# Kernel tuning notes

Measured on AMD Instinct MI355X. Metric: run time of the kernel, lower is better.

Reference implementation:

```python
import jax, jax.numpy as jnp
import numpy as np
from jax import lax

BIG = 1.0e6  # sentinel distance when a row contains no foreground pixel


def _dist1d(fg):
    """Exact 1D distance (in pixels) to nearest True along the last axis.

    fg: bool [..., W]. Returns float32 [..., W]; BIG where no True in the row.
    """
    W = fg.shape[-1]
    idx = jnp.arange(W, dtype=jnp.int32)
    # nearest foreground index to the left (inclusive)
    last = lax.cummax(jnp.where(fg, idx, -1), axis=fg.ndim - 1)
    d_left = jnp.where(last >= 0, (idx - last).astype(jnp.float32), BIG)
    # nearest foreground to the right: same scan on the reversed row
    fr = fg[..., ::-1]
    lastr = lax.cummax(jnp.where(fr, idx, -1), axis=fg.ndim - 1)
    d_right = jnp.where(lastr >= 0, (idx - lastr).astype(jnp.float32), BIG)[..., ::-1]
    return jnp.minimum(d_left, d_right)


def _edt2d(gt):
    """Exact Euclidean distance transform: distance from each pixel to the
    nearest gt==1 pixel (== scipy.distance_transform_edt(1-gt)).

    gt: [B, H, W] int. Returns float32 [B, H, W].
    Separable decomposition: D2(i,w) = min_j (d_row(j,w)^2 + (i-j)^2).
    """
    H = gt.shape[1]
    d_row = _dist1d(gt > 0)            # [B, H, W] 1D distances along rows
    dr2 = d_row * d_row                # squared row distances
    i = jnp.arange(H, dtype=jnp.float32)
    offs = (i[:, None] - i[None, :]) ** 2            # [Hi, Hj]
    # [B, Hi, Hj, W] = dr2 broadcast over i  +  (i-j)^2 broadcast over b, w
    d2 = jnp.min(dr2[:, None, :, :] + offs[None, :, :, None], axis=2)
    return jnp.sqrt(d2)


def setup_inputs() -> dict:
    key = jax.random.key(0)
    k1, k2 = jax.random.split(key)
    B, C, H, W = 8, 1, 256, 256
    logits = jax.random.normal(k1, (B, C, H, W), dtype=jnp.float32)
    target = jax.random.randint(k2, (B, C, H, W), 0, 2, dtype=jnp.int32)
    return {"logits": logits, "target": target}


def reference(logits, target):
    prob = jax.nn.sigmoid(logits)                      # [B, 1, H, W]
    D_gt = _edt2d(target[:, 0, :, :])[:, None, :, :]   # [B, 1, H, W]
    return jnp.mean(prob * D_gt)
```

## Files before the change

### kernel.cpp

```cpp
#include <hip/hip_runtime.h>


#define BIGF 1000000.0f
#define BIG2 (BIGF * BIGF)

constexpr int B = 8;
constexpr int H = 256;
constexpr int W = 256;
constexpr int NPIX = B * H * W;

__device__ __forceinline__ float block_reduce_sum_256(float v) {
    #pragma unroll
    for (int off = 32; off > 0; off >>= 1)
        v += __shfl_down(v, off, 64);
    __shared__ float s[4];
    const int lane = threadIdx.x & 63;
    const int wid  = threadIdx.x >> 6;
    if (lane == 0) s[wid] = v;
    __syncthreads();
    if (wid == 0) {
        v = (lane < 4) ? s[lane] : 0.0f;
        v += __shfl_down(v, 2, 64);
        v += __shfl_down(v, 1, 64);
    }
    return v;
}

__device__ __forceinline__ void upd16(const float4 m, float j0,
                                      float n0, float n1, float n2, float n3,
                                      float& b0, float& b1, float& b2, float& b3) {
    const float j1 = j0 + 1.0f, j2 = j0 + 2.0f, j3 = j0 + 3.0f;
    {
        const float c0 = fmaf(n0, j0, m.x), c1 = fmaf(n0, j1, m.y);
        const float c2 = fmaf(n0, j2, m.z), c3 = fmaf(n0, j3, m.w);
        b0 = fminf(b0, fminf(fminf(c0, c1), fminf(c2, c3)));
    }
    {
        const float c0 = fmaf(n1, j0, m.x), c1 = fmaf(n1, j1, m.y);
        const float c2 = fmaf(n1, j2, m.z), c3 = fmaf(n1, j3, m.w);
        b1 = fminf(b1, fminf(fminf(c0, c1), fminf(c2, c3)));
    }
    {
        const float c0 = fmaf(n2, j0, m.x), c1 = fmaf(n2, j1, m.y);
        const float c2 = fmaf(n2, j2, m.z), c3 = fmaf(n2, j3, m.w);
        b2 = fminf(b2, fminf(fminf(c0, c1), fminf(c2, c3)));
    }
    {
        const float c0 = fmaf(n3, j0, m.x), c1 = fmaf(n3, j1, m.y);
        const float c2 = fmaf(n3, j2, m.z), c3 = fmaf(n3, j3, m.w);
        b3 = fminf(b3, fminf(fminf(c0, c1), fminf(c2, c3)));
    }
}

__global__ __launch_bounds__(256) void row_dist_kernel(
        const int* __restrict__ target, float* __restrict__ dr2) {
    __shared__ float s_q[4][256];
    const int lane = threadIdx.x & 63;
    const int wv   = threadIdx.x >> 6;
    const int row  = (blockIdx.x << 2) + wv;

    const int4 tv = *(const int4*)(target + row * W + (lane << 2));
    const float fj0 = (float)(lane << 2);
    const float fj1 = fj0 + 1.0f, fj2 = fj0 + 2.0f, fj3 = fj0 + 3.0f;
    float4 q;
    q.x = fmaf(fj0, fj0, tv.x > 0 ? 0.0f : BIG2);
    q.y = fmaf(fj1, fj1, tv.y > 0 ? 0.0f : BIG2);
    q.z = fmaf(fj2, fj2, tv.z > 0 ? 0.0f : BIG2);
    q.w = fmaf(fj3, fj3, tv.w > 0 ? 0.0f : BIG2);
    *(float4*)&s_q[wv][lane << 2] = q;
    __syncthreads();

    const float w0f = (float)lane,         w1f = (float)(lane + 64);
    const float w2f = (float)(lane + 128), w3f = (float)(lane + 192);
    const float n0 = -2.0f * w0f, n1 = -2.0f * w1f;
    const float n2 = -2.0f * w2f, n3 = -2.0f * w3f;
    float b0 = 4e12f, b1 = 4e12f, b2 = 4e12f, b3 = 4e12f;

    float fj = 0.0f;
    #pragma unroll 4
    for (int jv = 0; jv < 64; ++jv, fj += 4.0f) {
        const float4 m = *(const float4*)&s_q[wv][jv << 2];
        upd16(m, fj, n0, n1, n2, n3, b0, b1, b2, b3);
    }

    const int base = row * W + lane;
    dr2[base]       = fmaf(w0f, w0f, b0);
    dr2[base + 64]  = fmaf(w1f, w1f, b1);
    dr2[base + 128] = fmaf(w2f, w2f, b2);
    dr2[base + 192] = fmaf(w3f, w3f, b3);
}

__global__ __launch_bounds__(256) void col_pass_kernel(
        const float* __restrict__ logits, const float* __restrict__ dr2,
        float* __restrict__ partials) {
    __shared__ float s_q[4][256];
    const int t  = threadIdx.x;
    const int b  = blockIdx.x >> 6;
    const int w0 = (blockIdx.x & 63) << 2;

    const float4 v  = *(const float4*)(dr2 + (b * H + t) * W + w0);
    const float fj  = (float)t;
    const float fj2 = fj * fj;
    s_q[0][t] = fj2 + v.x;
    s_q[1][t] = fj2 + v.y;
    s_q[2][t] = fj2 + v.z;
    s_q[3][t] = fj2 + v.w;
    __syncthreads();

    const int lane = t & 63;
    const int wv   = t >> 6;
    const float i0f = (float)lane,         i1f = (float)(lane + 64);
    const float i2f = (float)(lane + 128), i3f = (float)(lane + 192);
    const float n0 = -2.0f * i0f, n1 = -2.0f * i1f;
    const float n2 = -2.0f * i2f, n3 = -2.0f * i3f;
    float b0 = 4e12f, b1 = 4e12f, b2 = 4e12f, b3 = 4e12f;

    float fjv = 0.0f;
    #pragma unroll 4
    for (int jv = 0; jv < 64; ++jv, fjv += 4.0f) {
        const float4 m = *(const float4*)&s_q[wv][jv << 2];
        upd16(m, fjv, n0, n1, n2, n3, b0, b1, b2, b3);
    }

    const int wcol = w0 + wv;
    const int base = (b * H + lane) * W + wcol;
    float acc;
    {
        const float dist = sqrtf(fmaf(i0f, i0f, b0));
        const float x = logits[base];
        acc = dist / (1.0f + expf(-x));
    }
    {
        const float dist = sqrtf(fmaf(i1f, i1f, b1));
        const float x = logits[base + 64 * W];
        acc += dist / (1.0f + expf(-x));
    }
    {
        const float dist = sqrtf(fmaf(i2f, i2f, b2));
        const float x = logits[base + 128 * W];
        acc += dist / (1.0f + expf(-x));
    }
    {
        const float dist = sqrtf(fmaf(i3f, i3f, b3));
        const float x = logits[base + 192 * W];
        acc += dist / (1.0f + expf(-x));
    }

    const float s = block_reduce_sum_256(acc);
    if (t == 0) partials[blockIdx.x] = s;
}

__global__ __launch_bounds__(256) void final_reduce_kernel(
        const float* __restrict__ partials, float* __restrict__ out,
        int n, float scale) {
    float v = 0.0f;
    for (int idx = threadIdx.x; idx < n; idx += 256)
        v += partials[idx];
    v = block_reduce_sum_256(v);
    if (threadIdx.x == 0) out[0] = v * scale;
}

extern "C" void kernel_launch(void* const* d_in, const int* in_sizes, int n_in,
                              void* d_out, int out_size, void* d_ws, size_t ws_size,
                              hipStream_t stream) {
    const float* logits = (const float*)d_in[0];
    const int*   target = (const int*)d_in[1];

    float* dr2      = (float*)d_ws;
    float* partials = dr2 + NPIX;

    row_dist_kernel<<<B * H / 4, 256, 0, stream>>>(target, dr2);
    col_pass_kernel<<<B * W / 4, 256, 0, stream>>>(logits, dr2, partials);
    final_reduce_kernel<<<1, 256, 0, stream>>>(partials, (float*)d_out,
                                               B * W / 4, 1.0f / (float)NPIX);
}
```

Measured before the change: 74.56 us.

## Replace brute-force row pass with wave scans; split column min and fuse reduction

The row pass no longer does an O(W^2) min-plus search. It computes exact 1D nearest-foreground distances with wavefront prefix max/min scans (shfl_up/shfl_down), then writes the squared distances. The column pass now handles two columns per block and splits the j range across wave pairs, combining partial minima through shared memory. This doubles the block count and coalesces the logits loads as float2. The final reduce kernel is removed: each block atomically adds its scaled sum into the output, which the row kernel zeroes first. That relies on kernel ordering, and float atomics make the result order-nondeterministic.

```diff
diff --git a/kernel.cpp b/kernel.cpp
--- a/kernel.cpp
+++ b/kernel.cpp
@@ -3,6 +3,7 @@
 
 #define BIGF 1000000.0f
 #define BIG2 (BIGF * BIGF)
+#define BIGI (1 << 20)
 
 constexpr int B = 8;
 constexpr int H = 256;
@@ -24,6 +25,65 @@
         v += __shfl_down(v, 1, 64);
     }
     return v;
+}
+
+__global__ __launch_bounds__(256) void row_dist_kernel(
+        const int* __restrict__ target, float* __restrict__ dr2,
+        float* __restrict__ out) {
+    if (blockIdx.x == 0 && threadIdx.x == 0) out[0] = 0.0f;
+
+    const int lane = threadIdx.x & 63;
+    const int wv   = threadIdx.x >> 6;
+    const int row  = (blockIdx.x << 2) + wv;
+    const int p0   = lane << 2;
+
+    const int4 tv = *(const int4*)(target + row * W + p0);
+
+    const int l0 = (tv.x > 0) ? p0     : -1;
+    const int l1 = (tv.y > 0) ? p0 + 1 : l0;
+    const int l2 = (tv.z > 0) ? p0 + 2 : l1;
+    const int l3 = (tv.w > 0) ? p0 + 3 : l2;
+    int v = l3;
+    #pragma unroll
+    for (int off = 1; off < 64; off <<= 1) {
+        const int u = __shfl_up(v, off, 64);
+        if (lane >= off) v = max(v, u);
+    }
+    int exv = __shfl_up(v, 1, 64);
+    if (lane == 0) exv = -1;
+    const int last0 = max(exv, l0), last1 = max(exv, l1);
+    const int last2 = max(exv, l2), last3 = max(exv, l3);
+
+    const int r3 = (tv.w > 0) ? p0 + 3 : BIGI;
+    const int r2 = (tv.z > 0) ? p0 + 2 : r3;
+    const int r1 = (tv.y > 0) ? p0 + 1 : r2;
+    const int r0 = (tv.x > 0) ? p0     : r1;
+    int s = r0;
+    #pragma unroll
+    for (int off = 1; off < 64; off <<= 1) {
+        const int u = __shfl_down(s, off, 64);
+        if (lane < 64 - off) s = min(s, u);
+    }
+    int exs = __shfl_down(s, 1, 64);
+    if (lane == 63) exs = BIGI;
+    const int nxt0 = min(exs, r0), nxt1 = min(exs, r1);
+    const int nxt2 = min(exs, r2), nxt3 = min(exs, r3);
+
+    const int dl0 = (last0 >= 0) ? p0     - last0 : BIGI;
+    const int dl1 = (last1 >= 0) ? p0 + 1 - last1 : BIGI;
+    const int dl2 = (last2 >= 0) ? p0 + 2 - last2 : BIGI;
+    const int dl3 = (last3 >= 0) ? p0 + 3 - last3 : BIGI;
+    const int d0 = min(dl0, nxt0 - p0);
+    const int d1 = min(dl1, nxt1 - (p0 + 1));
+    const int d2 = min(dl2, nxt2 - (p0 + 2));
+    const int d3 = min(dl3, nxt3 - (p0 + 3));
+
+    float4 o;
+    o.x = (d0 < W) ? (float)(d0 * d0) : BIG2;
+    o.y = (d1 < W) ? (float)(d1 * d1) : BIG2;
+    o.z = (d2 < W) ? (float)(d2 * d2) : BIG2;
+    o.w = (d3 < W) ? (float)(d3 * d3) : BIG2;
+    *(float4*)(dr2 + row * W + p0) = o;
 }
 
 __device__ __forceinline__ void upd16(const float4 m, float j0,
@@ -52,112 +112,62 @@
     }
 }
 
-__global__ __launch_bounds__(256) void row_dist_kernel(
-        const int* __restrict__ target, float* __restrict__ dr2) {
-    __shared__ float s_q[4][256];
-    const int lane = threadIdx.x & 63;
-    const int wv   = threadIdx.x >> 6;
-    const int row  = (blockIdx.x << 2) + wv;
+__global__ __launch_bounds__(256) void col_pass_kernel(
+        const float* __restrict__ logits, const float* __restrict__ dr2,
+        float* __restrict__ out) {
+    __shared__ float s_q[2][256];
+    __shared__ float s_part[4][256];
 
-    const int4 tv = *(const int4*)(target + row * W + (lane << 2));
-    const float fj0 = (float)(lane << 2);
-    const float fj1 = fj0 + 1.0f, fj2 = fj0 + 2.0f, fj3 = fj0 + 3.0f;
-    float4 q;
-    q.x = fmaf(fj0, fj0, tv.x > 0 ? 0.0f : BIG2);
-    q.y = fmaf(fj1, fj1, tv.y > 0 ? 0.0f : BIG2);
-    q.z = fmaf(fj2, fj2, tv.z > 0 ? 0.0f : BIG2);
-    q.w = fmaf(fj3, fj3, tv.w > 0 ? 0.0f : BIG2);
-    *(float4*)&s_q[wv][lane << 2] = q;
+    const int t  = threadIdx.x;
+    const int b  = blockIdx.x >> 7;
+    const int w0 = (blockIdx.x & 127) << 1;
+
+    const float2 v  = *(const float2*)(dr2 + (b * H + t) * W + w0);
+    const float ft  = (float)t;
+    const float fj2 = ft * ft;
+    s_q[0][t] = fj2 + v.x;
+    s_q[1][t] = fj2 + v.y;
     __syncthreads();
 
-    const float w0f = (float)lane,         w1f = (float)(lane + 64);
-    const float w2f = (float)(lane + 128), w3f = (float)(lane + 192);
-    const float n0 = -2.0f * w0f, n1 = -2.0f * w1f;
-    const float n2 = -2.0f * w2f, n3 = -2.0f * w3f;
-    float b0 = 4e12f, b1 = 4e12f, b2 = 4e12f, b3 = 4e12f;
+    const int lane  = t & 63;
+    const int wv    = t >> 6;
+    const int c     = wv >> 1;
+    const int jbase = (wv & 1) << 7;
 
-    float fj = 0.0f;
-    #pragma unroll 4
-    for (int jv = 0; jv < 64; ++jv, fj += 4.0f) {
-        const float4 m = *(const float4*)&s_q[wv][jv << 2];
-        upd16(m, fj, n0, n1, n2, n3, b0, b1, b2, b3);
-    }
-
-    const int base = row * W + lane;
-    dr2[base]       = fmaf(w0f, w0f, b0);
-    dr2[base + 64]  = fmaf(w1f, w1f, b1);
-    dr2[base + 128] = fmaf(w2f, w2f, b2);
-    dr2[base + 192] = fmaf(w3f, w3f, b3);
-}
-
-__global__ __launch_bounds__(256) void col_pass_kernel(
-        const float* __restrict__ logits, const float* __restrict__ dr2,
-        float* __restrict__ partials) {
-    __shared__ float s_q[4][256];
-    const int t  = threadIdx.x;
-    const int b  = blockIdx.x >> 6;
-    const int w0 = (blockIdx.x & 63) << 2;
-
-    const float4 v  = *(const float4*)(dr2 + (b * H + t) * W + w0);
-    const float fj  = (float)t;
-    const float fj2 = fj * fj;
-    s_q[0][t] = fj2 + v.x;
-    s_q[1][t] = fj2 + v.y;
-    s_q[2][t] = fj2 + v.z;
-    s_q[3][t] = fj2 + v.w;
-    __syncthreads();
-
-    const int lane = t & 63;
-    const int wv   = t >> 6;
     const float i0f = (float)lane,         i1f = (float)(lane + 64);
     const float i2f = (float)(lane + 128), i3f = (float)(lane + 192);
     const float n0 = -2.0f * i0f, n1 = -2.0f * i1f;
     const float n2 = -2.0f * i2f, n3 = -2.0f * i3f;
     float b0 = 4e12f, b1 = 4e12f, b2 = 4e12f, b3 = 4e12f;
 
-    float fjv = 0.0f;
+    float fj = (float)jbase;
     #pragma unroll 4
-    for (int jv = 0; jv < 64; ++jv, fjv += 4.0f) {
-        const float4 m = *(const float4*)&s_q[wv][jv << 2];
-        upd16(m, fjv, n0, n1, n2, n3, b0, b1, b2, b3);
+    for (int jv = 0; jv < 32; ++jv, fj += 4.0f) {
+        const float4 m = *(const float4*)&s_q[c][jbase + (jv << 2)];
+        upd16(m, fj, n0, n1, n2, n3, b0, b1, b2, b3);
     }
 
-    const int wcol = w0 + wv;
-    const int base = (b * H + lane) * W + wcol;
+    s_part[wv][lane]       = b0;
+    s_part[wv][lane + 64]  = b1;
+    s_part[wv][lane + 128] = b2;
+    s_part[wv][lane + 192] = b3;
+    __syncthreads();
+
+    const float2 lg = *(const float2*)(logits + (b * H + t) * W + w0);
     float acc;
     {
-        const float dist = sqrtf(fmaf(i0f, i0f, b0));
-        const float x = logits[base];
-        acc = dist / (1.0f + expf(-x));
+        const float best = fminf(s_part[0][t], s_part[1][t]);
+        const float dist = sqrtf(fmaf(ft, ft, best));
+        acc = dist / (1.0f + expf(-lg.x));
     }
     {
-        const float dist = sqrtf(fmaf(i1f, i1f, b1));
-        const float x = logits[base + 64 * W];
-        acc += dist / (1.0f + expf(-x));
-    }
-    {
-        const float dist = sqrtf(fmaf(i2f, i2f, b2));
-        const float x = logits[base + 128 * W];
-        acc += dist / (1.0f + expf(-x));
-    }
-    {
-        const float dist = sqrtf(fmaf(i3f, i3f, b3));
-        const float x = logits[base + 192 * W];
-        acc += dist / (1.0f + expf(-x));
+        const float best = fminf(s_part[2][t], s_part[3][t]);
+        const float dist = sqrtf(fmaf(ft, ft, best));
+        acc += dist / (1.0f + expf(-lg.y));
     }
 
-    const float s = block_reduce_sum_256(acc);
-    if (t == 0) partials[blockIdx.x] = s;
-}
-
-__global__ __launch_bounds__(256) void final_reduce_kernel(
-        const float* __restrict__ partials, float* __restrict__ out,
-        int n, float scale) {
-    float v = 0.0f;
-    for (int idx = threadIdx.x; idx < n; idx += 256)
-        v += partials[idx];
-    v = block_reduce_sum_256(v);
-    if (threadIdx.x == 0) out[0] = v * scale;
+    const float sum = block_reduce_sum_256(acc);
+    if (t == 0) atomicAdd(out, sum * (1.0f / (float)NPIX));
 }
 
 extern "C" void kernel_launch(void* const* d_in, const int* in_sizes, int n_in,
@@ -165,12 +175,9 @@
                               hipStream_t stream) {
     const float* logits = (const float*)d_in[0];
     const int*   target = (const int*)d_in[1];
+    float*       out    = (float*)d_out;
+    float*       dr2    = (float*)d_ws;
 
-    float* dr2      = (float*)d_ws;
-    float* partials = dr2 + NPIX;
-
-    row_dist_kernel<<<B * H / 4, 256, 0, stream>>>(target, dr2);
-    col_pass_kernel<<<B * W / 4, 256, 0, stream>>>(logits, dr2, partials);
-    final_reduce_kernel<<<1, 256, 0, stream>>>(partials, (float*)d_out,
-                                               B * W / 4, 1.0f / (float)NPIX);
+    row_dist_kernel<<<B * H / 4, 256, 0, stream>>>(target, dr2, out);
+    col_pass_kernel<<<B * W / 2, 256, 0, stream>>>(logits, dr2, out);
 }
```

Measured after the change: 76.40 us (median of 2 runs). 2.5% more time.
